# Performance work log

Measured on AMD Instinct MI355X. Metric: run time of the kernel, lower is better.

The kernel has to match this reference:

```python
import jax, jax.numpy as jnp
import numpy as np

N = 1024
H = 128

def setup_inputs() -> dict:
    key = jax.random.key(0)
    ks = jax.random.split(key, 16)
    s = 1.0 / np.sqrt(H)
    inp = {
        "h": jax.random.normal(ks[0], (N, H), jnp.float32),
        "x": jax.random.normal(ks[1], (N, 2), jnp.float32),
        "batch": jnp.zeros((N,), jnp.int64),
        # Linear params stored as [in, out]
        "Wq": jax.random.normal(ks[2], (H, H), jnp.float32) * s,
        "bq": jnp.zeros((H,), jnp.float32),
        "Wk": jax.random.normal(ks[3], (H, H), jnp.float32) * s,
        "bk": jnp.zeros((H,), jnp.float32),
        "Wv": jax.random.normal(ks[4], (H, H), jnp.float32) * s,
        "bv": jnp.zeros((H,), jnp.float32),
        "We1": jax.random.normal(ks[5], (2, H), jnp.float32) * (1.0 / np.sqrt(2.0)),
        "be1": jnp.zeros((H,), jnp.float32),
        "We2": jax.random.normal(ks[6], (H, H), jnp.float32) * s,
        "be2": jnp.zeros((H,), jnp.float32),
        "Wc": jax.random.normal(ks[7], (H, 1), jnp.float32) * s,
        "bc": jnp.zeros((1,), jnp.float32),
    }
    return inp

def reference(h, x, batch, Wq, bq, Wk, bk, Wv, bv, We1, be1, We2, be2, Wc, bc):
    hidden = h.shape[-1]
    # pairwise relative coordinates: [N, N, 2]
    rel_x = x[:, None, :] - x[None, :, :]
    # edge MLP: Linear(2->H) -> ReLU -> Linear(H->H), [N, N, H]
    edge_feat = jax.nn.relu(rel_x @ We1 + be1) @ We2 + be2
    # attention: scaled dot-product over all pairs
    q = h @ Wq + bq
    k = h @ Wk + bk
    v = h @ Wv + bv
    attn_score = (q @ k.T) / jnp.sqrt(jnp.asarray(hidden, h.dtype))  # [N, N]
    attn_weight = jax.nn.softmax(attn_score, axis=-1)
    agg_h = attn_weight @ v  # [N, H]
    # coordinate update: per-pair scalar gate times rel_x, attn-weighted sum over j
    gate = edge_feat @ Wc + bc                     # [N, N, 1]
    delta_x = jnp.sum(attn_weight[:, :, None] * gate * rel_x, axis=1)  # [N, 2]
    return (h + agg_h, x + delta_x)
```

## Files before the change

### kernel.cpp

```cpp
#include <hip/hip_runtime.h>
#include <math.h>

#define NN 1024
#define HH 128

typedef _Float16 h2 __attribute__((ext_vector_type(2)));
typedef _Float16 h4 __attribute__((ext_vector_type(4)));
typedef _Float16 h8 __attribute__((ext_vector_type(8)));

__device__ inline float fdot2(h2 a, h2 b, float c) {
  return __builtin_amdgcn_fdot2(a, b, c, false);
}

__global__ __launch_bounds__(512) void qkv_kernel(
    const float* __restrict__ h, const float* __restrict__ x,
    const float* __restrict__ Wq, const float* __restrict__ bq,
    const float* __restrict__ Wk, const float* __restrict__ bk,
    const float* __restrict__ Wv, const float* __restrict__ bv,
    const float* __restrict__ We1,
    const float* __restrict__ We2, const float* __restrict__ be2,
    const float* __restrict__ Wc, const float* __restrict__ bc,
    float* __restrict__ q, _Float16* __restrict__ KP,
    _Float16* __restrict__ VP, float* __restrict__ Wc2,
    float* __restrict__ bc2) {
  const int t = threadIdx.x;

  if (blockIdx.x == 256) {
    if (t < HH) {
      float a = 0.f;
      for (int d = 0; d < HH; ++d) a = fmaf(We2[t * HH + d], Wc[d], a);
      Wc2[t] = a;
      if (t == 0) {
        float b = bc[0];
        for (int d = 0; d < HH; ++d) b = fmaf(be2[d], Wc[d], b);
        *bc2 = b;
      }
    }
    return;
  }

  __shared__ float4 hs4[HH];
  __shared__ float xsh[8];
  const int r0 = blockIdx.x * 4;
  if (t < HH) {
    hs4[t] = make_float4(h[(r0 + 0) * HH + t], h[(r0 + 1) * HH + t],
                         h[(r0 + 2) * HH + t], h[(r0 + 3) * HH + t]);
  }
  if (t >= HH && t < HH + 8) xsh[t - HH] = x[r0 * 2 + (t - HH)];
  __syncthreads();

  const int mat = t >> 7;
  const int col = t & 127;

  if (mat == 3) {
    const float w0 = We1[col], w1 = We1[HH + col];
    const int base = ((col >> 1) * (NN / 2) + (r0 >> 1)) * 8 + 4 + (col & 1);
#pragma unroll
    for (int rr = 0; rr < 4; ++rr) {
      float p = fmaf(xsh[2 * rr], w0, xsh[2 * rr + 1] * w1);
      KP[base + (rr >> 1) * 8 + (rr & 1) * 2] = (_Float16)p;
    }
    return;
  }

  const float* W = (mat == 0) ? Wq : (mat == 1) ? Wk : Wv;
  const float* B = (mat == 0) ? bq : (mat == 1) ? bk : bv;
  const float b = B[col];
  float a0 = b, a1 = b, a2 = b, a3 = b;
#pragma unroll 8
  for (int c = 0; c < HH; ++c) {
    float w = W[c * HH + col];
    float4 hv = hs4[c];
    a0 = fmaf(hv.x, w, a0);
    a1 = fmaf(hv.y, w, a1);
    a2 = fmaf(hv.z, w, a2);
    a3 = fmaf(hv.w, w, a3);
  }
  if (mat == 0) {
    const float scale = 0.08838834764831845f;
    q[(r0 + 0) * HH + col] = a0 * scale;
    q[(r0 + 1) * HH + col] = a1 * scale;
    q[(r0 + 2) * HH + col] = a2 * scale;
    q[(r0 + 3) * HH + col] = a3 * scale;
  } else if (mat == 1) {
    const int base = ((col >> 1) * (NN / 2) + (r0 >> 1)) * 8 + (col & 1);
    KP[base + 0] = (_Float16)a0;
    KP[base + 2] = (_Float16)a1;
    KP[base + 8] = (_Float16)a2;
    KP[base + 10] = (_Float16)a3;
  } else {
    const int base = ((r0 >> 2) * (HH / 2) + (col >> 1)) * 8 + (col & 1) * 2;
    VP[base + 0] = (_Float16)a0;
    VP[base + 1] = (_Float16)a1;
    VP[base + 4] = (_Float16)a2;
    VP[base + 5] = (_Float16)a3;
  }
}

__global__ __launch_bounds__(512) void attn_kernel(
    const float* __restrict__ h, const float* __restrict__ x,
    const float* __restrict__ q, const h8* __restrict__ KP,
    const h8* __restrict__ VP, const float* __restrict__ be1,
    const float* __restrict__ Wc2p, const float* __restrict__ bc2p,
    float* __restrict__ out) {
  __shared__ h8 qpp[HH / 2];
  __shared__ h2 ccs[HH / 2];
  __shared__ h4 wspi[NN / 2];
  __shared__ float xs[NN * 2];
  __shared__ float part[8][2][HH];
  __shared__ float red[6][8];

  const int i0 = blockIdx.x * 2, i1 = i0 + 1;
  const int tid = threadIdx.x;
  const int lane = tid & 63, wave = tid >> 6;

  if (tid < HH / 2) {
    const int u = tid;
    float2 qa = *(const float2*)(q + i0 * HH + 2 * u);
    float2 qb = *(const float2*)(q + i1 * HH + 2 * u);
    h8 kp = KP[u * (NN / 2) + (i0 >> 1)];
    float2 b1 = *(const float2*)(be1 + 2 * u);
    h8 a;
    a[0] = (_Float16)qa.x; a[1] = (_Float16)qa.y;
    a[2] = (_Float16)qb.x; a[3] = (_Float16)qb.y;
    a[4] = (_Float16)((float)kp[4] + b1.x);
    a[5] = (_Float16)((float)kp[5] + b1.y);
    a[6] = (_Float16)((float)kp[6] + b1.x);
    a[7] = (_Float16)((float)kp[7] + b1.y);
    qpp[u] = a;
    h2 c;
    c.x = (_Float16)Wc2p[2 * u];
    c.y = (_Float16)Wc2p[2 * u + 1];
    ccs[u] = c;
  }
  for (int j = tid; j < NN * 2; j += 512) xs[j] = x[j];
  const float bc2 = *bc2p;
  __syncthreads();

  const float xi0x = xs[2 * i0], xi0y = xs[2 * i0 + 1];
  const float xi1x = xs[2 * i1], xi1y = xs[2 * i1 + 1];
  const int j0 = 2 * tid, j1 = j0 + 1;
  const float xj0x = xs[2 * j0], xj0y = xs[2 * j0 + 1];
  const float xj1x = xs[2 * j1], xj1y = xs[2 * j1 + 1];
  const float rx00 = xi0x - xj0x, ry00 = xi0y - xj0y;
  const float rx01 = xi0x - xj1x, ry01 = xi0y - xj1y;
  const float rx10 = xi1x - xj0x, ry10 = xi1y - xj0y;
  const float rx11 = xi1x - xj1x, ry11 = xi1y - xj1y;

  h2 Z2;
  Z2.x = Z2.y = (_Float16)0;

  float s00 = 0.f, s01 = 0.f, s10 = 0.f, s11 = 0.f;
  float g00 = bc2, g01 = bc2, g10 = bc2, g11 = bc2;
  const h8* kptr = KP + tid;
  h8 kbuf[8];
#pragma unroll
  for (int p = 0; p < 8; ++p) kbuf[p] = kptr[p * (NN / 2)];
  for (int ub = 0; ub < HH / 2; ub += 8) {
#pragma unroll
    for (int p = 0; p < 8; ++p) {
      const int u = ub + p;
      h8 kp = kbuf[p];
      kbuf[p] = kptr[(u + 8) * (NN / 2)];
      h8 qp = qpp[u];
      h2 cc = ccs[u];
      h2 ka, kb, pj0, pj1, q0, q1, pi0, pi1;
      ka.x = kp[0]; ka.y = kp[1];
      kb.x = kp[2]; kb.y = kp[3];
      pj0.x = kp[4]; pj0.y = kp[5];
      pj1.x = kp[6]; pj1.y = kp[7];
      q0.x = qp[0]; q0.y = qp[1];
      q1.x = qp[2]; q1.y = qp[3];
      pi0.x = qp[4]; pi0.y = qp[5];
      pi1.x = qp[6]; pi1.y = qp[7];
      s00 = fdot2(q0, ka, s00);
      s01 = fdot2(q0, kb, s01);
      s10 = fdot2(q1, ka, s10);
      s11 = fdot2(q1, kb, s11);
      h2 t00 = __builtin_elementwise_max(pi0 - pj0, Z2);
      h2 t01 = __builtin_elementwise_max(pi0 - pj1, Z2);
      h2 t10 = __builtin_elementwise_max(pi1 - pj0, Z2);
      h2 t11 = __builtin_elementwise_max(pi1 - pj1, Z2);
      g00 = fdot2(t00, cc, g00);
      g01 = fdot2(t01, cc, g01);
      g10 = fdot2(t10, cc, g10);
      g11 = fdot2(t11, cc, g11);
    }
  }
  const float e00 = __expf(s00), e01 = __expf(s01);
  const float e10 = __expf(s10), e11 = __expf(s11);
  {
    h4 w;
    w[0] = (_Float16)e00; w[1] = (_Float16)e01;
    w[2] = (_Float16)e10; w[3] = (_Float16)e11;
    wspi[tid] = w;
  }
  const float wg00 = e00 * g00, wg01 = e01 * g01;
  const float wg10 = e10 * g10, wg11 = e11 * g11;
  float l0 = e00 + e01, l1 = e10 + e11;
  float dx0 = fmaf(wg00, rx00, wg01 * rx01);
  float dy0 = fmaf(wg00, ry00, wg01 * ry01);
  float dx1 = fmaf(wg10, rx10, wg11 * rx11);
  float dy1 = fmaf(wg10, ry10, wg11 * ry11);
#pragma unroll
  for (int off = 32; off > 0; off >>= 1) {
    l0 += __shfl_down(l0, off);
    l1 += __shfl_down(l1, off);
    dx0 += __shfl_down(dx0, off);
    dy0 += __shfl_down(dy0, off);
    dx1 += __shfl_down(dx1, off);
    dy1 += __shfl_down(dy1, off);
  }
  if (lane == 0) {
    red[0][wave] = l0;  red[1][wave] = l1;
    red[2][wave] = dx0; red[3][wave] = dy0;
    red[4][wave] = dx1; red[5][wave] = dy1;
  }

  {
    const int j4b = wave * 32;
    const h8* wsp8 = (const h8*)wspi;
    const h8* vptr = VP + j4b * (HH / 2) + lane;
    h8 vbuf[8];
#pragma unroll
    for (int p = 0; p < 8; ++p) vbuf[p] = vptr[p * (HH / 2)];
    float a0x = 0.f, a0y = 0.f, a1x = 0.f, a1y = 0.f;
    for (int jb = 0; jb < 32; jb += 8) {
#pragma unroll
      for (int p = 0; p < 8; ++p) {
        const int j4 = j4b + jb + p;
        h8 vv = vbuf[p];
        vbuf[p] = vptr[(jb + 8 + p) * (HH / 2)];
        h8 wj = wsp8[j4];
        h2 w0a, w1a, w0b, w1b, v0a, v1a, v0b, v1b;
        w0a.x = wj[0]; w0a.y = wj[1];
        w1a.x = wj[2]; w1a.y = wj[3];
        w0b.x = wj[4]; w0b.y = wj[5];
        w1b.x = wj[6]; w1b.y = wj[7];
        v0a.x = vv[0]; v0a.y = vv[1];
        v1a.x = vv[2]; v1a.y = vv[3];
        v0b.x = vv[4]; v0b.y = vv[5];
        v1b.x = vv[6]; v1b.y = vv[7];
        a0x = fdot2(w0a, v0a, a0x);
        a0x = fdot2(w0b, v0b, a0x);
        a0y = fdot2(w0a, v1a, a0y);
        a0y = fdot2(w0b, v1b, a0y);
        a1x = fdot2(w1a, v0a, a1x);
        a1x = fdot2(w1b, v0b, a1x);
        a1y = fdot2(w1a, v1a, a1y);
        a1y = fdot2(w1b, v1b, a1y);
      }
    }
    part[wave][0][2 * lane] = a0x;
    part[wave][0][2 * lane + 1] = a0y;
    part[wave][1][2 * lane] = a1x;
    part[wave][1][2 * lane + 1] = a1y;
  }
  __syncthreads();

  float sum0 = 0.f, sum1 = 0.f;
#pragma unroll
  for (int w = 0; w < 8; ++w) { sum0 += red[0][w]; sum1 += red[1][w]; }
  const float inv0 = 1.f / sum0, inv1 = 1.f / sum1;

  if (tid == 0) {
    float DX0 = 0.f, DY0 = 0.f, DX1 = 0.f, DY1 = 0.f;
#pragma unroll
    for (int w = 0; w < 8; ++w) {
      DX0 += red[2][w]; DY0 += red[3][w];
      DX1 += red[4][w]; DY1 += red[5][w];
    }
    out[NN * HH + i0 * 2 + 0] = xi0x + DX0 * inv0;
    out[NN * HH + i0 * 2 + 1] = xi0y + DY0 * inv0;
    out[NN * HH + i1 * 2 + 0] = xi1x + DX1 * inv1;
    out[NN * HH + i1 * 2 + 1] = xi1y + DY1 * inv1;
  }

  if (tid < 256) {
    const int r = tid >> 7, c = tid & 127;
    float s = 0.f;
#pragma unroll
    for (int g = 0; g < 8; ++g) s += part[g][r][c];
    out[(i0 + r) * HH + c] = h[(i0 + r) * HH + c] + s * (r ? inv1 : inv0);
  }
}

extern "C" void kernel_launch(void* const* d_in, const int* in_sizes, int n_in,
                              void* d_out, int out_size, void* d_ws, size_t ws_size,
                              hipStream_t stream) {
  const float* h   = (const float*)d_in[0];
  const float* x   = (const float*)d_in[1];
  const float* Wq  = (const float*)d_in[3];
  const float* bq  = (const float*)d_in[4];
  const float* Wk  = (const float*)d_in[5];
  const float* bk  = (const float*)d_in[6];
  const float* Wv  = (const float*)d_in[7];
  const float* bv  = (const float*)d_in[8];
  const float* We1 = (const float*)d_in[9];
  const float* be1 = (const float*)d_in[10];
  const float* We2 = (const float*)d_in[11];
  const float* be2 = (const float*)d_in[12];
  const float* Wc  = (const float*)d_in[13];
  const float* bc  = (const float*)d_in[14];
  float* out = (float*)d_out;

  float* wsf = (float*)d_ws;
  float* q = wsf;
  _Float16* KP = (_Float16*)(wsf + NN * HH);
  _Float16* VP = KP + (HH / 2) * (NN / 2) * 8;
  float* Wc2 = (float*)(VP + (NN / 4) * (HH / 2) * 8);
  float* bc2 = Wc2 + HH;

  qkv_kernel<<<257, 512, 0, stream>>>(h, x, Wq, bq, Wk, bk, Wv, bv, We1, We2,
                                      be2, Wc, bc, q, KP, VP, Wc2, bc2);
  attn_kernel<<<512, 512, 0, stream>>>(h, x, q, (const h8*)KP, (const h8*)VP,
                                       be1, Wc2, bc2, out);
}
```

Baseline: 108.3 us.

## Process four query rows per attention block to reuse K and V loads

Each attention block now handles four query rows instead of two, so every K and V fragment read from global memory feeds twice as many dot products, and the grid is halved to 256 blocks. The cost targeted is the repeated global/L2 traffic for K and V across blocks. In exchange each thread holds more accumulators and the block uses more shared memory, which may lower occupancy, and 256 blocks may leave some compute units underused. The unroll factor in the QKV projection loop is also raised.

Measured after the change: 108.5 us. About the same (+0.1%).

```diff
diff --git a/kernel.cpp b/kernel.cpp
--- a/kernel.cpp
+++ b/kernel.cpp
@@ -67,7 +67,7 @@
   const float* B = (mat == 0) ? bq : (mat == 1) ? bk : bv;
   const float b = B[col];
   float a0 = b, a1 = b, a2 = b, a3 = b;
-#pragma unroll 8
+#pragma unroll 16
   for (int c = 0; c < HH; ++c) {
     float w = W[c * HH + col];
     float4 hv = hs4[c];
@@ -103,22 +103,24 @@
     const h8* __restrict__ VP, const float* __restrict__ be1,
     const float* __restrict__ Wc2p, const float* __restrict__ bc2p,
     float* __restrict__ out) {
-  __shared__ h8 qpp[HH / 2];
+  __shared__ h8 qps[2][HH / 2];
   __shared__ h2 ccs[HH / 2];
-  __shared__ h4 wspi[NN / 2];
+  __shared__ h4 wspA[NN / 2];
+  __shared__ h4 wspB[NN / 2];
   __shared__ float xs[NN * 2];
-  __shared__ float part[8][2][HH];
-  __shared__ float red[6][8];
-
-  const int i0 = blockIdx.x * 2, i1 = i0 + 1;
+  __shared__ float part[8][4][HH];
+  __shared__ float red[12][8];
+
+  const int i0 = blockIdx.x * 4;
   const int tid = threadIdx.x;
   const int lane = tid & 63, wave = tid >> 6;
 
-  if (tid < HH / 2) {
-    const int u = tid;
-    float2 qa = *(const float2*)(q + i0 * HH + 2 * u);
-    float2 qb = *(const float2*)(q + i1 * HH + 2 * u);
-    h8 kp = KP[u * (NN / 2) + (i0 >> 1)];
+  if (tid < HH) {
+    const int s = tid >> 6, u = tid & 63;
+    const int iA = i0 + 2 * s, iB = iA + 1;
+    float2 qa = *(const float2*)(q + iA * HH + 2 * u);
+    float2 qb = *(const float2*)(q + iB * HH + 2 * u);
+    h8 kp = KP[u * (NN / 2) + (iA >> 1)];
     float2 b1 = *(const float2*)(be1 + 2 * u);
     h8 a;
     a[0] = (_Float16)qa.x; a[1] = (_Float16)qa.y;
@@ -127,31 +129,35 @@
     a[5] = (_Float16)((float)kp[5] + b1.y);
     a[6] = (_Float16)((float)kp[6] + b1.x);
     a[7] = (_Float16)((float)kp[7] + b1.y);
-    qpp[u] = a;
-    h2 c;
-    c.x = (_Float16)Wc2p[2 * u];
-    c.y = (_Float16)Wc2p[2 * u + 1];
-    ccs[u] = c;
+    qps[s][u] = a;
+    if (s == 0) {
+      h2 c;
+      c.x = (_Float16)Wc2p[2 * u];
+      c.y = (_Float16)Wc2p[2 * u + 1];
+      ccs[u] = c;
+    }
   }
   for (int j = tid; j < NN * 2; j += 512) xs[j] = x[j];
   const float bc2 = *bc2p;
   __syncthreads();
 
-  const float xi0x = xs[2 * i0], xi0y = xs[2 * i0 + 1];
-  const float xi1x = xs[2 * i1], xi1y = xs[2 * i1 + 1];
+  float xix[4], xiy[4];
+#pragma unroll
+  for (int r = 0; r < 4; ++r) {
+    xix[r] = xs[2 * (i0 + r)];
+    xiy[r] = xs[2 * (i0 + r) + 1];
+  }
   const int j0 = 2 * tid, j1 = j0 + 1;
   const float xj0x = xs[2 * j0], xj0y = xs[2 * j0 + 1];
   const float xj1x = xs[2 * j1], xj1y = xs[2 * j1 + 1];
-  const float rx00 = xi0x - xj0x, ry00 = xi0y - xj0y;
-  const float rx01 = xi0x - xj1x, ry01 = xi0y - xj1y;
-  const float rx10 = xi1x - xj0x, ry10 = xi1y - xj0y;
-  const float rx11 = xi1x - xj1x, ry11 = xi1y - xj1y;
 
   h2 Z2;
   Z2.x = Z2.y = (_Float16)0;
 
-  float s00 = 0.f, s01 = 0.f, s10 = 0.f, s11 = 0.f;
-  float g00 = bc2, g01 = bc2, g10 = bc2, g11 = bc2;
+  float sc[8];
+  float gt[8];
+#pragma unroll
+  for (int z = 0; z < 8; ++z) { sc[z] = 0.f; gt[z] = bc2; }
   const h8* kptr = KP + tid;
   h8 kbuf[8];
 #pragma unroll
@@ -162,85 +168,102 @@
       const int u = ub + p;
       h8 kp = kbuf[p];
       kbuf[p] = kptr[(u + 8) * (NN / 2)];
-      h8 qp = qpp[u];
-      h2 cc = ccs[u];
-      h2 ka, kb, pj0, pj1, q0, q1, pi0, pi1;
+      h2 ka, kb, pj0, pj1, cc;
       ka.x = kp[0]; ka.y = kp[1];
       kb.x = kp[2]; kb.y = kp[3];
       pj0.x = kp[4]; pj0.y = kp[5];
       pj1.x = kp[6]; pj1.y = kp[7];
-      q0.x = qp[0]; q0.y = qp[1];
-      q1.x = qp[2]; q1.y = qp[3];
-      pi0.x = qp[4]; pi0.y = qp[5];
-      pi1.x = qp[6]; pi1.y = qp[7];
-      s00 = fdot2(q0, ka, s00);
-      s01 = fdot2(q0, kb, s01);
-      s10 = fdot2(q1, ka, s10);
-      s11 = fdot2(q1, kb, s11);
-      h2 t00 = __builtin_elementwise_max(pi0 - pj0, Z2);
-      h2 t01 = __builtin_elementwise_max(pi0 - pj1, Z2);
-      h2 t10 = __builtin_elementwise_max(pi1 - pj0, Z2);
-      h2 t11 = __builtin_elementwise_max(pi1 - pj1, Z2);
-      g00 = fdot2(t00, cc, g00);
-      g01 = fdot2(t01, cc, g01);
-      g10 = fdot2(t10, cc, g10);
-      g11 = fdot2(t11, cc, g11);
-    }
-  }
-  const float e00 = __expf(s00), e01 = __expf(s01);
-  const float e10 = __expf(s10), e11 = __expf(s11);
+      cc = ccs[u];
+#pragma unroll
+      for (int s = 0; s < 2; ++s) {
+        h8 qp = qps[s][u];
+        h2 q0, q1, pi0, pi1;
+        q0.x = qp[0]; q0.y = qp[1];
+        q1.x = qp[2]; q1.y = qp[3];
+        pi0.x = qp[4]; pi0.y = qp[5];
+        pi1.x = qp[6]; pi1.y = qp[7];
+        sc[4 * s + 0] = fdot2(q0, ka, sc[4 * s + 0]);
+        sc[4 * s + 1] = fdot2(q0, kb, sc[4 * s + 1]);
+        sc[4 * s + 2] = fdot2(q1, ka, sc[4 * s + 2]);
+        sc[4 * s + 3] = fdot2(q1, kb, sc[4 * s + 3]);
+        h2 t00 = __builtin_elementwise_max(pi0 - pj0, Z2);
+        h2 t01 = __builtin_elementwise_max(pi0 - pj1, Z2);
+        h2 t10 = __builtin_elementwise_max(pi1 - pj0, Z2);
+        h2 t11 = __builtin_elementwise_max(pi1 - pj1, Z2);
+        gt[4 * s + 0] = fdot2(t00, cc, gt[4 * s + 0]);
+        gt[4 * s + 1] = fdot2(t01, cc, gt[4 * s + 1]);
+        gt[4 * s + 2] = fdot2(t10, cc, gt[4 * s + 2]);
+        gt[4 * s + 3] = fdot2(t11, cc, gt[4 * s + 3]);
+      }
+    }
+  }
+  float e[8];
+#pragma unroll
+  for (int z = 0; z < 8; ++z) e[z] = __expf(sc[z]);
   {
-    h4 w;
-    w[0] = (_Float16)e00; w[1] = (_Float16)e01;
-    w[2] = (_Float16)e10; w[3] = (_Float16)e11;
-    wspi[tid] = w;
-  }
-  const float wg00 = e00 * g00, wg01 = e01 * g01;
-  const float wg10 = e10 * g10, wg11 = e11 * g11;
-  float l0 = e00 + e01, l1 = e10 + e11;
-  float dx0 = fmaf(wg00, rx00, wg01 * rx01);
-  float dy0 = fmaf(wg00, ry00, wg01 * ry01);
-  float dx1 = fmaf(wg10, rx10, wg11 * rx11);
-  float dy1 = fmaf(wg10, ry10, wg11 * ry11);
+    h4 wA, wB;
+    wA[0] = (_Float16)e[0]; wA[1] = (_Float16)e[1];
+    wA[2] = (_Float16)e[2]; wA[3] = (_Float16)e[3];
+    wB[0] = (_Float16)e[4]; wB[1] = (_Float16)e[5];
+    wB[2] = (_Float16)e[6]; wB[3] = (_Float16)e[7];
+    wspA[tid] = wA;
+    wspB[tid] = wB;
+  }
+  float lr[4], dxr[4], dyr[4];
+#pragma unroll
+  for (int r = 0; r < 4; ++r) {
+    const float w0 = e[2 * r] * gt[2 * r];
+    const float w1 = e[2 * r + 1] * gt[2 * r + 1];
+    lr[r] = e[2 * r] + e[2 * r + 1];
+    dxr[r] = fmaf(w0, xix[r] - xj0x, w1 * (xix[r] - xj1x));
+    dyr[r] = fmaf(w0, xiy[r] - xj0y, w1 * (xiy[r] - xj1y));
+  }
 #pragma unroll
   for (int off = 32; off > 0; off >>= 1) {
-    l0 += __shfl_down(l0, off);
-    l1 += __shfl_down(l1, off);
-    dx0 += __shfl_down(dx0, off);
-    dy0 += __shfl_down(dy0, off);
-    dx1 += __shfl_down(dx1, off);
-    dy1 += __shfl_down(dy1, off);
+#pragma unroll
+    for (int r = 0; r < 4; ++r) {
+      lr[r] += __shfl_down(lr[r], off);
+      dxr[r] += __shfl_down(dxr[r], off);
+      dyr[r] += __shfl_down(dyr[r], off);
+    }
   }
   if (lane == 0) {
-    red[0][wave] = l0;  red[1][wave] = l1;
-    red[2][wave] = dx0; red[3][wave] = dy0;
-    red[4][wave] = dx1; red[5][wave] = dy1;
+#pragma unroll
+    for (int r = 0; r < 4; ++r) {
+      red[r][wave] = lr[r];
+      red[4 + r][wave] = dxr[r];
+      red[8 + r][wave] = dyr[r];
+    }
   }
 
   {
     const int j4b = wave * 32;
-    const h8* wsp8 = (const h8*)wspi;
+    const h8* wA8 = (const h8*)wspA;
+    const h8* wB8 = (const h8*)wspB;
     const h8* vptr = VP + j4b * (HH / 2) + lane;
     h8 vbuf[8];
 #pragma unroll
     for (int p = 0; p < 8; ++p) vbuf[p] = vptr[p * (HH / 2)];
     float a0x = 0.f, a0y = 0.f, a1x = 0.f, a1y = 0.f;
+    float a2x = 0.f, a2y = 0.f, a3x = 0.f, a3y = 0.f;
     for (int jb = 0; jb < 32; jb += 8) {
 #pragma unroll
       for (int p = 0; p < 8; ++p) {
         const int j4 = j4b + jb + p;
         h8 vv = vbuf[p];
         vbuf[p] = vptr[(jb + 8 + p) * (HH / 2)];
-        h8 wj = wsp8[j4];
-        h2 w0a, w1a, w0b, w1b, v0a, v1a, v0b, v1b;
-        w0a.x = wj[0]; w0a.y = wj[1];
-        w1a.x = wj[2]; w1a.y = wj[3];
-        w0b.x = wj[4]; w0b.y = wj[5];
-        w1b.x = wj[6]; w1b.y = wj[7];
+        h8 wjA = wA8[j4];
+        h8 wjB = wB8[j4];
+        h2 v0a, v1a, v0b, v1b;
         v0a.x = vv[0]; v0a.y = vv[1];
         v1a.x = vv[2]; v1a.y = vv[3];
         v0b.x = vv[4]; v0b.y = vv[5];
         v1b.x = vv[6]; v1b.y = vv[7];
+        h2 w0a, w1a, w0b, w1b;
+        w0a.x = wjA[0]; w0a.y = wjA[1];
+        w1a.x = wjA[2]; w1a.y = wjA[3];
+        w0b.x = wjA[4]; w0b.y = wjA[5];
+        w1b.x = wjA[6]; w1b.y = wjA[7];
         a0x = fdot2(w0a, v0a, a0x);
         a0x = fdot2(w0b, v0b, a0x);
         a0y = fdot2(w0a, v1a, a0y);
@@ -249,39 +272,61 @@
         a1x = fdot2(w1b, v0b, a1x);
         a1y = fdot2(w1a, v1a, a1y);
         a1y = fdot2(w1b, v1b, a1y);
+        h2 w2a, w3a, w2b, w3b;
+        w2a.x = wjB[0]; w2a.y = wjB[1];
+        w3a.x = wjB[2]; w3a.y = wjB[3];
+        w2b.x = wjB[4]; w2b.y = wjB[5];
+        w3b.x = wjB[6]; w3b.y = wjB[7];
+        a2x = fdot2(w2a, v0a, a2x);
+        a2x = fdot2(w2b, v0b, a2x);
+        a2y = fdot2(w2a, v1a, a2y);
+        a2y = fdot2(w2b, v1b, a2y);
+        a3x = fdot2(w3a, v0a, a3x);
+        a3x = fdot2(w3b, v0b, a3x);
+        a3y = fdot2(w3a, v1a, a3y);
+        a3y = fdot2(w3b, v1b, a3y);
       }
     }
     part[wave][0][2 * lane] = a0x;
     part[wave][0][2 * lane + 1] = a0y;
     part[wave][1][2 * lane] = a1x;
     part[wave][1][2 * lane + 1] = a1y;
+    part[wave][2][2 * lane] = a2x;
+    part[wave][2][2 * lane + 1] = a2y;
+    part[wave][3][2 * lane] = a3x;
+    part[wave][3][2 * lane + 1] = a3y;
   }
   __syncthreads();
 
-  float sum0 = 0.f, sum1 = 0.f;
-#pragma unroll
-  for (int w = 0; w < 8; ++w) { sum0 += red[0][w]; sum1 += red[1][w]; }
-  const float inv0 = 1.f / sum0, inv1 = 1.f / sum1;
+  float inv[4];
+#pragma unroll
+  for (int r = 0; r < 4; ++r) {
+    float s = 0.f;
+#pragma unroll
+    for (int w = 0; w < 8; ++w) s += red[r][w];
+    inv[r] = 1.f / s;
+  }
 
   if (tid == 0) {
-    float DX0 = 0.f, DY0 = 0.f, DX1 = 0.f, DY1 = 0.f;
-#pragma unroll
-    for (int w = 0; w < 8; ++w) {
-      DX0 += red[2][w]; DY0 += red[3][w];
-      DX1 += red[4][w]; DY1 += red[5][w];
-    }
-    out[NN * HH + i0 * 2 + 0] = xi0x + DX0 * inv0;
-    out[NN * HH + i0 * 2 + 1] = xi0y + DY0 * inv0;
-    out[NN * HH + i1 * 2 + 0] = xi1x + DX1 * inv1;
-    out[NN * HH + i1 * 2 + 1] = xi1y + DY1 * inv1;
-  }
-
-  if (tid < 256) {
+#pragma unroll
+    for (int r = 0; r < 4; ++r) {
+      float DX = 0.f, DY = 0.f;
+#pragma unroll
+      for (int w = 0; w < 8; ++w) {
+        DX += red[4 + r][w];
+        DY += red[8 + r][w];
+      }
+      out[NN * HH + (i0 + r) * 2 + 0] = xix[r] + DX * inv[r];
+      out[NN * HH + (i0 + r) * 2 + 1] = xiy[r] + DY * inv[r];
+    }
+  }
+
+  {
     const int r = tid >> 7, c = tid & 127;
     float s = 0.f;
 #pragma unroll
     for (int g = 0; g < 8; ++g) s += part[g][r][c];
-    out[(i0 + r) * HH + c] = h[(i0 + r) * HH + c] + s * (r ? inv1 : inv0);
+    out[(i0 + r) * HH + c] = h[(i0 + r) * HH + c] + s * inv[r];
   }
 }
 
@@ -313,6 +358,6 @@
 
   qkv_kernel<<<257, 512, 0, stream>>>(h, x, Wq, bq, Wk, bk, Wv, bv, We1, We2,
                                       be2, Wc, bc, q, KP, VP, Wc2, bc2);
-  attn_kernel<<<512, 512, 0, stream>>>(h, x, q, (const h8*)KP, (const h8*)VP,
+  attn_kernel<<<256, 512, 0, stream>>>(h, x, q, (const h8*)KP, (const h8*)VP,
                                        be1, Wc2, bc2, out);
 }
```
